# Performance work log

Hardware: AMD Instinct MI355X
Metric: run time of the kernel (lower is better)

## Reference

```python
import jax, jax.numpy as jnp
import numpy as np

N_NODES = 50000
N_EDGES = 800000
D_IN = 64
D_HID = 64
N_LAYERS = 3


def setup_inputs() -> dict:
    key = jax.random.key(0)
    ks = jax.random.split(key, 3 + 2 * N_LAYERS)
    x = jax.random.normal(ks[0], (N_NODES, D_IN), dtype=jnp.float32)
    edge_index = jax.random.randint(ks[1], (2, N_EDGES), 0, N_NODES, dtype=jnp.int64)
    edge_weight = jax.random.uniform(ks[2], (N_EDGES,), dtype=jnp.float32)
    inp = {"x": x, "edge_index": edge_index, "edge_weight": edge_weight}
    dims = [(D_IN, D_HID)] + [(D_HID, D_HID)] * (N_LAYERS - 1)
    for i, (din, dout) in enumerate(dims):
        # Glorot-style init like PyG GCNConv
        scale = jnp.sqrt(6.0 / (din + dout)).astype(jnp.float32)
        inp[f"W{i}"] = jax.random.uniform(ks[3 + 2 * i], (din, dout), dtype=jnp.float32, minval=-1.0, maxval=1.0) * scale
        inp[f"b{i}"] = jnp.zeros((dout,), dtype=jnp.float32)
    return inp


def _gcn_norm(edge_index, edge_weight, num_nodes, dtype):
    # Add self-loops with weight 1, then symmetric normalization (PyG gcn_norm).
    loop = jnp.arange(num_nodes)
    src = jnp.concatenate([edge_index[0], loop])
    dst = jnp.concatenate([edge_index[1], loop])
    w = jnp.concatenate([edge_weight, jnp.ones((num_nodes,), dtype=dtype)])
    deg = jax.ops.segment_sum(w, dst, num_segments=num_nodes)  # [N]
    dinv = jnp.where(deg > 0, jax.lax.rsqrt(deg), jnp.zeros_like(deg))
    norm = dinv[src] * w * dinv[dst]  # [E+N]
    return src, dst, norm


def reference(x, edge_index, edge_weight, W0, b0, W1, b1, W2, b2):
    N = x.shape[0]
    src, dst, norm = _gcn_norm(edge_index, edge_weight, N, x.dtype)
    for W, b in ((W0, b0), (W1, b1), (W2, b2)):
        h = x @ W                                   # [N, dout] linear first (PyG)
        msg = h[src] * norm[:, None]                # gather + scale per edge
        x = jax.ops.segment_sum(msg, dst, num_segments=N) + b  # scatter-add + bias
        x = jax.nn.relu(x)
    return x
```

## Files before the change

### kernel.cpp

```cpp
#include <hip/hip_runtime.h>

#define NN 50000
#define NE 800000
#define D  64
#define NB 782
#define NBLK 256
#define CHUNK 3125
#define CAP 1536
#define CAPTOT (NB * CAP)

__device__ __forceinline__ float blo(unsigned u) { return __uint_as_float(u << 16); }
__device__ __forceinline__ float bhi(unsigned u) { return __uint_as_float(u & 0xFFFF0000u); }
__device__ __forceinline__ unsigned short f2b(float f) {
    unsigned u = __float_as_uint(f);
    return (unsigned short)((u + 0x7FFFu + ((u >> 16) & 1u)) >> 16);
}

__global__ void k_init(int* __restrict__ cursor) {
    int i = blockIdx.x * blockDim.x + threadIdx.x;
    if (i < NB) cursor[i] = i * CAP;
}

__global__ __launch_bounds__(256) void p12(const int* __restrict__ src,
        const int* __restrict__ dst, const float* __restrict__ w,
        int* __restrict__ cursor, int2* __restrict__ stage) {
    __shared__ unsigned se[CHUNK];
    __shared__ float    sw[CHUNK];
    __shared__ int      lh[NB];
    int t = threadIdx.x;
    for (int i = t; i < NB; i += 256) lh[i] = 0;
    __syncthreads();
    int e0 = blockIdx.x * CHUNK;
    for (int i = t; i < CHUNK; i += 256) {
        int e = e0 + i;
        unsigned d = (unsigned)dst[e];
        unsigned s = (unsigned)src[e];
        float wv = w[e];
        unsigned pk = 0xFFFFFFFFu;
        if (d < NN) {
            pk = (s & 0xFFFFu) | ((d & 63u) << 16) | ((d >> 6) << 22);
            atomicAdd(&lh[d >> 6], 1);
        }
        se[i] = pk;
        sw[i] = wv;
    }
    __syncthreads();
    for (int i = t; i < NB; i += 256) {
        int c = lh[i];
        lh[i] = c ? atomicAdd(&cursor[i], c) : 0;
    }
    __syncthreads();
    for (int i = t; i < CHUNK; i += 256) {
        unsigned pk = se[i];
        if (pk != 0xFFFFFFFFu) {
            int bucket = (int)(pk >> 22);
            int pos = atomicAdd(&lh[bucket], 1);
            if (pos < (bucket + 1) * CAP)
                stage[pos] = make_int2((int)(pk & 0x3FFFFFu), __float_as_int(sw[i]));
        }
    }
}

__global__ __launch_bounds__(256) void p3_sort(const int2* __restrict__ stage,
        const int* __restrict__ cursor, int2* __restrict__ csr,
        int* __restrict__ row_ptr, int* __restrict__ row_deg, float* __restrict__ dinv) {
    __shared__ int   hist[64];
    __shared__ int   cur[64];
    __shared__ float wsum[64];
    int b = blockIdx.x, t = threadIdx.x;
    int g0 = b * CAP, g1 = cursor[b];
    if (t < 64) { hist[t] = 0; wsum[t] = 0.f; }
    __syncthreads();
    for (int j = g0 + t; j < g1; j += 256) {
        int2 pk = stage[j];
        int r = (pk.x >> 16) & 63;
        atomicAdd(&hist[r], 1);
        atomicAdd(&wsum[r], __int_as_float(pk.y));
    }
    __syncthreads();
    if (t == 0) {
        int s = g0;
        for (int r = 0; r < 64; ++r) { cur[r] = s; s += hist[r]; }
    }
    __syncthreads();
    if (t < 64) {
        int n = b * 64 + t;
        if (n < NN) {
            row_ptr[n] = cur[t];
            row_deg[n] = hist[t];
            dinv[n] = rsqrtf(wsum[t] + 1.0f);
        }
    }
    __syncthreads();
    for (int j = g0 + t; j < g1; j += 256) {
        int2 pk = stage[j];
        int r = (pk.x >> 16) & 63;
        int pos = atomicAdd(&cur[r], 1);
        csr[pos] = make_int2(pk.x & 0xFFFF, pk.y);
    }
}

__global__ __launch_bounds__(256) void gemm_pre_kernel(const float* __restrict__ x,
        const float* __restrict__ W, const float* __restrict__ dinv,
        unsigned short* __restrict__ hp) {
    __shared__ float xs[16][64];
    int t = threadIdx.x;
    int base = blockIdx.x * 16;
    for (int idx = t; idx < 16 * 64; idx += 256)
        xs[idx >> 6][idx & 63] = x[(size_t)(base + (idx >> 6)) * 64 + (idx & 63)];
    __syncthreads();
    int col = t & 63, rq = t >> 6;
    float wc[64];
#pragma unroll
    for (int k = 0; k < 64; ++k) wc[k] = W[k * 64 + col];
    float acc0 = 0.f, acc1 = 0.f, acc2 = 0.f, acc3 = 0.f;
#pragma unroll
    for (int k = 0; k < 64; ++k) {
        float wk = wc[k];
        acc0 += xs[rq     ][k] * wk;
        acc1 += xs[rq +  4][k] * wk;
        acc2 += xs[rq +  8][k] * wk;
        acc3 += xs[rq + 12][k] * wk;
    }
    int r = base + rq;
    hp[(size_t)(r     ) * 64 + col] = f2b(dinv[r     ] * acc0);
    hp[(size_t)(r +  4) * 64 + col] = f2b(dinv[r +  4] * acc1);
    hp[(size_t)(r +  8) * 64 + col] = f2b(dinv[r +  8] * acc2);
    hp[(size_t)(r + 12) * 64 + col] = f2b(dinv[r + 12] * acc3);
}

__device__ __forceinline__ float4 gather_row(int n, int fq, int qbase,
        const int* __restrict__ row_ptr, const int* __restrict__ row_deg,
        const int2* __restrict__ csr, const uint2* __restrict__ hp64) {
    int s0 = row_ptr[n], s1 = s0 + row_deg[n];
    uint2 self = hp64[(size_t)n * 16 + fq];
    float ax = blo(self.x), ay = bhi(self.x), az = blo(self.y), aw = bhi(self.y);
    float bx = 0.f, by = 0.f, bz = 0.f, bw = 0.f;
    for (int base = s0; base < s1; base += 16) {
        int j = base + fq;
        int si = 0; float wl = 0.f;
        if (j < s1) {
            int2 pk = csr[j];
            si = pk.x;
            wl = __int_as_float(pk.y);
        }
        int m = s1 - base; if (m > 16) m = 16;
        int jj = 0;
        for (; jj + 4 <= m; jj += 4) {
            int a0 = __shfl(si, qbase + jj + 0); float w0 = __shfl(wl, qbase + jj + 0);
            int a1 = __shfl(si, qbase + jj + 1); float w1 = __shfl(wl, qbase + jj + 1);
            int a2 = __shfl(si, qbase + jj + 2); float w2 = __shfl(wl, qbase + jj + 2);
            int a3 = __shfl(si, qbase + jj + 3); float w3 = __shfl(wl, qbase + jj + 3);
            uint2 u0 = hp64[(size_t)a0 * 16 + fq];
            uint2 u1 = hp64[(size_t)a1 * 16 + fq];
            uint2 u2 = hp64[(size_t)a2 * 16 + fq];
            uint2 u3 = hp64[(size_t)a3 * 16 + fq];
            ax += w0 * blo(u0.x); ay += w0 * bhi(u0.x); az += w0 * blo(u0.y); aw += w0 * bhi(u0.y);
            bx += w1 * blo(u1.x); by += w1 * bhi(u1.x); bz += w1 * blo(u1.y); bw += w1 * bhi(u1.y);
            ax += w2 * blo(u2.x); ay += w2 * bhi(u2.x); az += w2 * blo(u2.y); aw += w2 * bhi(u2.y);
            bx += w3 * blo(u3.x); by += w3 * bhi(u3.x); bz += w3 * blo(u3.y); bw += w3 * bhi(u3.y);
        }
        for (; jj < m; ++jj) {
            int a0 = __shfl(si, qbase + jj); float w0 = __shfl(wl, qbase + jj);
            uint2 u0 = hp64[(size_t)a0 * 16 + fq];
            ax += w0 * blo(u0.x); ay += w0 * bhi(u0.x); az += w0 * blo(u0.y); aw += w0 * bhi(u0.y);
        }
    }
    return make_float4(ax + bx, ay + by, az + bz, aw + bw);
}

__global__ __launch_bounds__(256) void fused_kernel(const int* __restrict__ row_ptr,
        const int* __restrict__ row_deg, const int2* __restrict__ csr,
        const float* __restrict__ dinv, const uint2* __restrict__ hp_cur,
        const float* __restrict__ bias, const float* __restrict__ Wn,
        unsigned short* __restrict__ hp_next) {
    __shared__ float ys[16][64];
    int t = threadIdx.x;
    int lane = t & 63, q = lane >> 4, fq = lane & 15;
    int ni = ((t >> 6) << 2) + q;
    int n = blockIdx.x * 16 + ni;
    float4 g = gather_row(n, fq, q << 4, row_ptr, row_deg, csr, hp_cur);
    float dv = dinv[n];
    float4 bb = ((const float4*)bias)[fq];
    float4 y;
    y.x = fmaxf(dv * g.x + bb.x, 0.f);
    y.y = fmaxf(dv * g.y + bb.y, 0.f);
    y.z = fmaxf(dv * g.z + bb.z, 0.f);
    y.w = fmaxf(dv * g.w + bb.w, 0.f);
    ((float4*)ys[ni])[fq] = y;
    __syncthreads();
    int col = lane, rq = t >> 6;
    float wc[64];
#pragma unroll
    for (int k = 0; k < 64; ++k) wc[k] = Wn[k * 64 + col];
    float a0 = 0.f, a1 = 0.f, a2 = 0.f, a3 = 0.f;
#pragma unroll
    for (int k = 0; k < 64; ++k) {
        float wk = wc[k];
        a0 += ys[rq     ][k] * wk;
        a1 += ys[rq +  4][k] * wk;
        a2 += ys[rq +  8][k] * wk;
        a3 += ys[rq + 12][k] * wk;
    }
    int r = blockIdx.x * 16 + rq;
    hp_next[(size_t)(r     ) * 64 + col] = f2b(dinv[r     ] * a0);
    hp_next[(size_t)(r +  4) * 64 + col] = f2b(dinv[r +  4] * a1);
    hp_next[(size_t)(r +  8) * 64 + col] = f2b(dinv[r +  8] * a2);
    hp_next[(size_t)(r + 12) * 64 + col] = f2b(dinv[r + 12] * a3);
}

__global__ __launch_bounds__(256) void final_kernel(const int* __restrict__ row_ptr,
        const int* __restrict__ row_deg, const int2* __restrict__ csr,
        const float* __restrict__ dinv, const uint2* __restrict__ hp_cur,
        const float* __restrict__ bias, float* __restrict__ out) {
    int t = threadIdx.x;
    int lane = t & 63, q = lane >> 4, fq = lane & 15;
    int n = blockIdx.x * 16 + ((t >> 6) << 2) + q;
    float4 g = gather_row(n, fq, q << 4, row_ptr, row_deg, csr, hp_cur);
    float dv = dinv[n];
    float4 bb = ((const float4*)bias)[fq];
    float4 r;
    r.x = fmaxf(dv * g.x + bb.x, 0.f);
    r.y = fmaxf(dv * g.y + bb.y, 0.f);
    r.z = fmaxf(dv * g.z + bb.z, 0.f);
    r.w = fmaxf(dv * g.w + bb.w, 0.f);
    ((float4*)out)[(size_t)n * 16 + fq] = r;
}

extern "C" void kernel_launch(void* const* d_in, const int* in_sizes, int n_in,
                              void* d_out, int out_size, void* d_ws, size_t ws_size,
                              hipStream_t stream) {
    const float* x  = (const float*)d_in[0];
    const int*   ei = (const int*)d_in[1];
    const float* ew = (const float*)d_in[2];
    const float* W0 = (const float*)d_in[3];
    const float* b0 = (const float*)d_in[4];
    const float* W1 = (const float*)d_in[5];
    const float* b1 = (const float*)d_in[6];
    const float* W2 = (const float*)d_in[7];
    const float* b2 = (const float*)d_in[8];
    float*       out = (float*)d_out;

    const int* src = ei;
    const int* dst = ei + NE;

    int2*  stage   = (int2*)d_ws;
    int2*  csr     = stage + CAPTOT;
    int*   cursor  = (int*)(csr + CAPTOT);
    int*   row_ptr = cursor + NB;
    int*   row_deg = row_ptr + NN;
    float* dinv    = (float*)(row_deg + NN);
    unsigned short* hpA = (unsigned short*)(dinv + NN);
    unsigned short* hpB = hpA + (size_t)NN * 64;

    k_init<<<1, 1024, 0, stream>>>(cursor);
    p12<<<NBLK, 256, 0, stream>>>(src, dst, ew, cursor, stage);
    p3_sort<<<NB, 256, 0, stream>>>(stage, cursor, csr, row_ptr, row_deg, dinv);

    gemm_pre_kernel<<<NN / 16, 256, 0, stream>>>(x, W0, dinv, hpA);
    fused_kernel<<<NN / 16, 256, 0, stream>>>(row_ptr, row_deg, csr, dinv,
            (const uint2*)hpA, b0, W1, hpB);
    fused_kernel<<<NN / 16, 256, 0, stream>>>(row_ptr, row_deg, csr, dinv,
            (const uint2*)hpB, b1, W2, hpA);
    final_kernel<<<NN / 16, 256, 0, stream>>>(row_ptr, row_deg, csr, dinv,
            (const uint2*)hpA, b2, out);
}
```

Baseline: 201.0 us.

## Slice features into 8-wide column panels, pack CSR to 4 bytes, split gather/GEMM

Stores the bf16 feature matrix as 8 column slices of 8 features each, so every gather block works on one slice whose working set (50000 nodes × 16 bytes) is more likely to stay in cache. The CSR entry packs the 16-bit local source index and a bf16 edge weight into one 32-bit word, halving index traffic. The fused gather+GEMM kernel is split into separate gather and GEMM kernels, which adds launches and an intermediate bf16 round trip. Edge weights are now rounded to bf16, which lowers precision, and the stage read is clamped to bucket capacity.

```diff
diff --git a/kernel.cpp b/kernel.cpp
--- a/kernel.cpp
+++ b/kernel.cpp
@@ -2,7 +2,6 @@
 
 #define NN 50000
 #define NE 800000
-#define D  64
 #define NB 782
 #define NBLK 256
 #define CHUNK 3125
@@ -62,13 +61,16 @@
 }
 
 __global__ __launch_bounds__(256) void p3_sort(const int2* __restrict__ stage,
-        const int* __restrict__ cursor, int2* __restrict__ csr,
+        const int* __restrict__ cursor, unsigned* __restrict__ csr4,
         int* __restrict__ row_ptr, int* __restrict__ row_deg, float* __restrict__ dinv) {
     __shared__ int   hist[64];
     __shared__ int   cur[64];
     __shared__ float wsum[64];
     int b = blockIdx.x, t = threadIdx.x;
-    int g0 = b * CAP, g1 = cursor[b];
+    int g0 = b * CAP;
+    int g1 = cursor[b];
+    int gmax = g0 + CAP;
+    if (g1 > gmax) g1 = gmax;
     if (t < 64) { hist[t] = 0; wsum[t] = 0.f; }
     __syncthreads();
     for (int j = g0 + t; j < g1; j += 256) {
@@ -96,11 +98,12 @@
         int2 pk = stage[j];
         int r = (pk.x >> 16) & 63;
         int pos = atomicAdd(&cur[r], 1);
-        csr[pos] = make_int2(pk.x & 0xFFFF, pk.y);
-    }
-}
-
-__global__ __launch_bounds__(256) void gemm_pre_kernel(const float* __restrict__ x,
+        csr4[pos] = (unsigned)(pk.x & 0xFFFF) |
+                    ((unsigned)f2b(__int_as_float(pk.y)) << 16);
+    }
+}
+
+__global__ __launch_bounds__(256) void gemm0_kernel(const float* __restrict__ x,
         const float* __restrict__ W, const float* __restrict__ dinv,
         unsigned short* __restrict__ hp) {
     __shared__ float xs[16][64];
@@ -113,118 +116,135 @@
     float wc[64];
 #pragma unroll
     for (int k = 0; k < 64; ++k) wc[k] = W[k * 64 + col];
-    float acc0 = 0.f, acc1 = 0.f, acc2 = 0.f, acc3 = 0.f;
+    float a0 = 0.f, a1 = 0.f, a2 = 0.f, a3 = 0.f;
 #pragma unroll
     for (int k = 0; k < 64; ++k) {
         float wk = wc[k];
-        acc0 += xs[rq     ][k] * wk;
-        acc1 += xs[rq +  4][k] * wk;
-        acc2 += xs[rq +  8][k] * wk;
-        acc3 += xs[rq + 12][k] * wk;
+        a0 += xs[rq     ][k] * wk;
+        a1 += xs[rq +  4][k] * wk;
+        a2 += xs[rq +  8][k] * wk;
+        a3 += xs[rq + 12][k] * wk;
     }
     int r = base + rq;
-    hp[(size_t)(r     ) * 64 + col] = f2b(dinv[r     ] * acc0);
-    hp[(size_t)(r +  4) * 64 + col] = f2b(dinv[r +  4] * acc1);
-    hp[(size_t)(r +  8) * 64 + col] = f2b(dinv[r +  8] * acc2);
-    hp[(size_t)(r + 12) * 64 + col] = f2b(dinv[r + 12] * acc3);
-}
-
-__device__ __forceinline__ float4 gather_row(int n, int fq, int qbase,
-        const int* __restrict__ row_ptr, const int* __restrict__ row_deg,
-        const int2* __restrict__ csr, const uint2* __restrict__ hp64) {
-    int s0 = row_ptr[n], s1 = s0 + row_deg[n];
-    uint2 self = hp64[(size_t)n * 16 + fq];
-    float ax = blo(self.x), ay = bhi(self.x), az = blo(self.y), aw = bhi(self.y);
-    float bx = 0.f, by = 0.f, bz = 0.f, bw = 0.f;
-    for (int base = s0; base < s1; base += 16) {
-        int j = base + fq;
-        int si = 0; float wl = 0.f;
-        if (j < s1) {
-            int2 pk = csr[j];
-            si = pk.x;
-            wl = __int_as_float(pk.y);
-        }
-        int m = s1 - base; if (m > 16) m = 16;
-        int jj = 0;
-        for (; jj + 4 <= m; jj += 4) {
-            int a0 = __shfl(si, qbase + jj + 0); float w0 = __shfl(wl, qbase + jj + 0);
-            int a1 = __shfl(si, qbase + jj + 1); float w1 = __shfl(wl, qbase + jj + 1);
-            int a2 = __shfl(si, qbase + jj + 2); float w2 = __shfl(wl, qbase + jj + 2);
-            int a3 = __shfl(si, qbase + jj + 3); float w3 = __shfl(wl, qbase + jj + 3);
-            uint2 u0 = hp64[(size_t)a0 * 16 + fq];
-            uint2 u1 = hp64[(size_t)a1 * 16 + fq];
-            uint2 u2 = hp64[(size_t)a2 * 16 + fq];
-            uint2 u3 = hp64[(size_t)a3 * 16 + fq];
-            ax += w0 * blo(u0.x); ay += w0 * bhi(u0.x); az += w0 * blo(u0.y); aw += w0 * bhi(u0.y);
-            bx += w1 * blo(u1.x); by += w1 * bhi(u1.x); bz += w1 * blo(u1.y); bw += w1 * bhi(u1.y);
-            ax += w2 * blo(u2.x); ay += w2 * bhi(u2.x); az += w2 * blo(u2.y); aw += w2 * bhi(u2.y);
-            bx += w3 * blo(u3.x); by += w3 * bhi(u3.x); bz += w3 * blo(u3.y); bw += w3 * bhi(u3.y);
-        }
-        for (; jj < m; ++jj) {
-            int a0 = __shfl(si, qbase + jj); float w0 = __shfl(wl, qbase + jj);
-            uint2 u0 = hp64[(size_t)a0 * 16 + fq];
-            ax += w0 * blo(u0.x); ay += w0 * bhi(u0.x); az += w0 * blo(u0.y); aw += w0 * bhi(u0.y);
-        }
-    }
-    return make_float4(ax + bx, ay + by, az + bz, aw + bw);
-}
-
-__global__ __launch_bounds__(256) void fused_kernel(const int* __restrict__ row_ptr,
-        const int* __restrict__ row_deg, const int2* __restrict__ csr,
-        const float* __restrict__ dinv, const uint2* __restrict__ hp_cur,
-        const float* __restrict__ bias, const float* __restrict__ Wn,
-        unsigned short* __restrict__ hp_next) {
-    __shared__ float ys[16][64];
-    int t = threadIdx.x;
-    int lane = t & 63, q = lane >> 4, fq = lane & 15;
-    int ni = ((t >> 6) << 2) + q;
-    int n = blockIdx.x * 16 + ni;
-    float4 g = gather_row(n, fq, q << 4, row_ptr, row_deg, csr, hp_cur);
-    float dv = dinv[n];
-    float4 bb = ((const float4*)bias)[fq];
-    float4 y;
-    y.x = fmaxf(dv * g.x + bb.x, 0.f);
-    y.y = fmaxf(dv * g.y + bb.y, 0.f);
-    y.z = fmaxf(dv * g.z + bb.z, 0.f);
-    y.w = fmaxf(dv * g.w + bb.w, 0.f);
-    ((float4*)ys[ni])[fq] = y;
-    __syncthreads();
-    int col = lane, rq = t >> 6;
+    size_t pbase = (size_t)(col >> 3) * NN * 8 + (col & 7);
+    hp[pbase + (size_t)(r     ) * 8] = f2b(dinv[r     ] * a0);
+    hp[pbase + (size_t)(r +  4) * 8] = f2b(dinv[r +  4] * a1);
+    hp[pbase + (size_t)(r +  8) * 8] = f2b(dinv[r +  8] * a2);
+    hp[pbase + (size_t)(r + 12) * 8] = f2b(dinv[r + 12] * a3);
+}
+
+__global__ __launch_bounds__(256) void gemmn_kernel(const unsigned short* __restrict__ y,
+        const float* __restrict__ W, const float* __restrict__ dinv,
+        unsigned short* __restrict__ hp) {
+    __shared__ float xs[16][64];
+    int t = threadIdx.x;
+    int base = blockIdx.x * 16;
+    for (int idx = t; idx < 16 * 64; idx += 256) {
+        int node = base + (idx >> 6), f = idx & 63;
+        xs[idx >> 6][f] = blo((unsigned)y[(size_t)(f >> 3) * NN * 8 + (size_t)node * 8 + (f & 7)]);
+    }
+    __syncthreads();
+    int col = t & 63, rq = t >> 6;
     float wc[64];
 #pragma unroll
-    for (int k = 0; k < 64; ++k) wc[k] = Wn[k * 64 + col];
+    for (int k = 0; k < 64; ++k) wc[k] = W[k * 64 + col];
     float a0 = 0.f, a1 = 0.f, a2 = 0.f, a3 = 0.f;
 #pragma unroll
     for (int k = 0; k < 64; ++k) {
         float wk = wc[k];
-        a0 += ys[rq     ][k] * wk;
-        a1 += ys[rq +  4][k] * wk;
-        a2 += ys[rq +  8][k] * wk;
-        a3 += ys[rq + 12][k] * wk;
-    }
-    int r = blockIdx.x * 16 + rq;
-    hp_next[(size_t)(r     ) * 64 + col] = f2b(dinv[r     ] * a0);
-    hp_next[(size_t)(r +  4) * 64 + col] = f2b(dinv[r +  4] * a1);
-    hp_next[(size_t)(r +  8) * 64 + col] = f2b(dinv[r +  8] * a2);
-    hp_next[(size_t)(r + 12) * 64 + col] = f2b(dinv[r + 12] * a3);
-}
-
-__global__ __launch_bounds__(256) void final_kernel(const int* __restrict__ row_ptr,
-        const int* __restrict__ row_deg, const int2* __restrict__ csr,
-        const float* __restrict__ dinv, const uint2* __restrict__ hp_cur,
+        a0 += xs[rq     ][k] * wk;
+        a1 += xs[rq +  4][k] * wk;
+        a2 += xs[rq +  8][k] * wk;
+        a3 += xs[rq + 12][k] * wk;
+    }
+    int r = base + rq;
+    size_t pbase = (size_t)(col >> 3) * NN * 8 + (col & 7);
+    hp[pbase + (size_t)(r     ) * 8] = f2b(dinv[r     ] * a0);
+    hp[pbase + (size_t)(r +  4) * 8] = f2b(dinv[r +  4] * a1);
+    hp[pbase + (size_t)(r +  8) * 8] = f2b(dinv[r +  8] * a2);
+    hp[pbase + (size_t)(r + 12) * 8] = f2b(dinv[r + 12] * a3);
+}
+
+__device__ __forceinline__ float2 gather_body(int n, int gl, int gbase,
+        const int* __restrict__ row_ptr, const int* __restrict__ row_deg,
+        const unsigned* __restrict__ csr4, const unsigned* __restrict__ hps) {
+    int s0 = row_ptr[n], cnt = row_deg[n];
+    unsigned self = hps[n * 4 + gl];
+    float ax = blo(self), ay = bhi(self);
+    float bx = 0.f, by = 0.f;
+    int base = 0;
+    for (; base + 4 <= cnt; base += 4) {
+        unsigned meta = csr4[s0 + base + gl];
+        unsigned m0 = __shfl(meta, gbase + 0);
+        unsigned m1 = __shfl(meta, gbase + 1);
+        unsigned m2 = __shfl(meta, gbase + 2);
+        unsigned m3 = __shfl(meta, gbase + 3);
+        unsigned u0 = hps[(m0 & 0xFFFFu) * 4 + gl];
+        unsigned u1 = hps[(m1 & 0xFFFFu) * 4 + gl];
+        unsigned u2 = hps[(m2 & 0xFFFFu) * 4 + gl];
+        unsigned u3 = hps[(m3 & 0xFFFFu) * 4 + gl];
+        float w0 = __uint_as_float(m0 & 0xFFFF0000u);
+        float w1 = __uint_as_float(m1 & 0xFFFF0000u);
+        float w2 = __uint_as_float(m2 & 0xFFFF0000u);
+        float w3 = __uint_as_float(m3 & 0xFFFF0000u);
+        ax += w0 * blo(u0); ay += w0 * bhi(u0);
+        bx += w1 * blo(u1); by += w1 * bhi(u1);
+        ax += w2 * blo(u2); ay += w2 * bhi(u2);
+        bx += w3 * blo(u3); by += w3 * bhi(u3);
+    }
+    int rem = cnt - base;
+    if (rem > 0) {
+        unsigned meta = (gl < rem) ? csr4[s0 + base + gl] : 0u;
+        for (int jj = 0; jj < rem; ++jj) {
+            unsigned mm = __shfl(meta, gbase + jj);
+            unsigned u = hps[(mm & 0xFFFFu) * 4 + gl];
+            float w = __uint_as_float(mm & 0xFFFF0000u);
+            ax += w * blo(u); ay += w * bhi(u);
+        }
+    }
+    return make_float2(ax + bx, ay + by);
+}
+
+__global__ __launch_bounds__(256) void gather_mid(const int* __restrict__ row_ptr,
+        const int* __restrict__ row_deg, const unsigned* __restrict__ csr4,
+        const float* __restrict__ dinv, const unsigned* __restrict__ hp,
+        const float* __restrict__ bias, unsigned* __restrict__ y) {
+    int t = threadIdx.x;
+    int s = blockIdx.x & 7;
+    int nb = blockIdx.x >> 3;
+    int lane = t & 63;
+    int g = lane >> 2, gl = lane & 3;
+    int n = nb * 64 + ((t >> 6) << 4) + g;
+    if (n >= NN) return;
+    const unsigned* hps = hp + (size_t)s * NN * 4;
+    float2 acc = gather_body(n, gl, g << 2, row_ptr, row_deg, csr4, hps);
+    float dv = dinv[n];
+    float2 bb = ((const float2*)bias)[s * 4 + gl];
+    float rx = fmaxf(dv * acc.x + bb.x, 0.f);
+    float ry = fmaxf(dv * acc.y + bb.y, 0.f);
+    y[(size_t)s * NN * 4 + (size_t)n * 4 + gl] =
+        (unsigned)f2b(rx) | ((unsigned)f2b(ry) << 16);
+}
+
+__global__ __launch_bounds__(256) void gather_final(const int* __restrict__ row_ptr,
+        const int* __restrict__ row_deg, const unsigned* __restrict__ csr4,
+        const float* __restrict__ dinv, const unsigned* __restrict__ hp,
         const float* __restrict__ bias, float* __restrict__ out) {
     int t = threadIdx.x;
-    int lane = t & 63, q = lane >> 4, fq = lane & 15;
-    int n = blockIdx.x * 16 + ((t >> 6) << 2) + q;
-    float4 g = gather_row(n, fq, q << 4, row_ptr, row_deg, csr, hp_cur);
+    int s = blockIdx.x & 7;
+    int nb = blockIdx.x >> 3;
+    int lane = t & 63;
+    int g = lane >> 2, gl = lane & 3;
+    int n = nb * 64 + ((t >> 6) << 4) + g;
+    if (n >= NN) return;
+    const unsigned* hps = hp + (size_t)s * NN * 4;
+    float2 acc = gather_body(n, gl, g << 2, row_ptr, row_deg, csr4, hps);
     float dv = dinv[n];
-    float4 bb = ((const float4*)bias)[fq];
-    float4 r;
-    r.x = fmaxf(dv * g.x + bb.x, 0.f);
-    r.y = fmaxf(dv * g.y + bb.y, 0.f);
-    r.z = fmaxf(dv * g.z + bb.z, 0.f);
-    r.w = fmaxf(dv * g.w + bb.w, 0.f);
-    ((float4*)out)[(size_t)n * 16 + fq] = r;
+    float2 bb = ((const float2*)bias)[s * 4 + gl];
+    float2 r;
+    r.x = fmaxf(dv * acc.x + bb.x, 0.f);
+    r.y = fmaxf(dv * acc.y + bb.y, 0.f);
+    ((float2*)out)[(size_t)n * 32 + s * 4 + gl] = r;
 }
 
 extern "C" void kernel_launch(void* const* d_in, const int* in_sizes, int n_in,
@@ -244,24 +264,26 @@
     const int* src = ei;
     const int* dst = ei + NE;
 
-    int2*  stage   = (int2*)d_ws;
-    int2*  csr     = stage + CAPTOT;
-    int*   cursor  = (int*)(csr + CAPTOT);
-    int*   row_ptr = cursor + NB;
-    int*   row_deg = row_ptr + NN;
-    float* dinv    = (float*)(row_deg + NN);
-    unsigned short* hpA = (unsigned short*)(dinv + NN);
-    unsigned short* hpB = hpA + (size_t)NN * 64;
+    int2*     stage   = (int2*)d_ws;
+    unsigned* csr4    = (unsigned*)(stage + CAPTOT);
+    int*      cursor  = (int*)(csr4 + CAPTOT);
+    int*      row_ptr = cursor + NB;
+    int*      row_deg = row_ptr + NN;
+    float*    dinv    = (float*)(row_deg + NN);
+    unsigned short* hp = (unsigned short*)(dinv + NN);
+    unsigned short* y  = hp + (size_t)NN * 64;
 
     k_init<<<1, 1024, 0, stream>>>(cursor);
     p12<<<NBLK, 256, 0, stream>>>(src, dst, ew, cursor, stage);
-    p3_sort<<<NB, 256, 0, stream>>>(stage, cursor, csr, row_ptr, row_deg, dinv);
-
-    gemm_pre_kernel<<<NN / 16, 256, 0, stream>>>(x, W0, dinv, hpA);
-    fused_kernel<<<NN / 16, 256, 0, stream>>>(row_ptr, row_deg, csr, dinv,
-            (const uint2*)hpA, b0, W1, hpB);
-    fused_kernel<<<NN / 16, 256, 0, stream>>>(row_ptr, row_deg, csr, dinv,
-            (const uint2*)hpB, b1, W2, hpA);
-    final_kernel<<<NN / 16, 256, 0, stream>>>(row_ptr, row_deg, csr, dinv,
-            (const uint2*)hpA, b2, out);
-}
+    p3_sort<<<NB, 256, 0, stream>>>(stage, cursor, csr4, row_ptr, row_deg, dinv);
+
+    gemm0_kernel<<<NN / 16, 256, 0, stream>>>(x, W0, dinv, hp);
+    gather_mid<<<NB * 8, 256, 0, stream>>>(row_ptr, row_deg, csr4, dinv,
+            (const unsigned*)hp, b0, (unsigned*)y);
+    gemmn_kernel<<<NN / 16, 256, 0, stream>>>(y, W1, dinv, hp);
+    gather_mid<<<NB * 8, 256, 0, stream>>>(row_ptr, row_deg, csr4, dinv,
+            (const unsigned*)hp, b1, (unsigned*)y);
+    gemmn_kernel<<<NN / 16, 256, 0, stream>>>(y, W2, dinv, hp);
+    gather_final<<<NB * 8, 256, 0, stream>>>(row_ptr, row_deg, csr4, dinv,
+            (const unsigned*)hp, b2, out);
+}
```

New measurement: 269.3 us. +34.0%, slower.
